# Kernel tuning notes

Hardware: AMD Instinct MI355X
Metric: run time of the kernel (lower is better)

The kernel has to match this reference:

```python
import jax, jax.numpy as jnp
import numpy as np

N_NODES = 50000
N_EDGES = 800000
N_GRAPHS = 256
F_IN = 75  # num_features_xd


def _lin_params(key, fan_in, fan_out):
    kw, kb = jax.random.split(key)
    s = 1.0 / np.sqrt(fan_in)
    W = jax.random.uniform(kw, (fan_in, fan_out), jnp.float32, -s, s)
    b = jax.random.uniform(kb, (fan_out,), jnp.float32, -s, s)
    return W, b


def setup_inputs() -> dict:
    key = jax.random.key(0)
    ks = jax.random.split(key, 8)
    x = jax.random.normal(ks[0], (N_NODES, F_IN), jnp.float32)
    edge_index = jax.random.randint(ks[1], (2, N_EDGES), 0, N_NODES, jnp.int32)
    batch = jnp.sort(jax.random.randint(ks[2], (N_NODES,), 0, N_GRAPHS, jnp.int32))
    W1, b1 = _lin_params(ks[3], F_IN, F_IN)            # conv1: 75 -> 75
    W2, b2 = _lin_params(ks[4], F_IN, 2 * F_IN)        # conv2: 75 -> 150
    W3, b3 = _lin_params(ks[5], 2 * F_IN, 4 * F_IN)    # conv3: 150 -> 300
    Wg1, bg1 = _lin_params(ks[6], 4 * F_IN, 1024)      # fc_g1: 300 -> 1024
    Wg2, bg2 = _lin_params(ks[7], 1024, 128)           # fc_g2: 1024 -> 128
    return dict(x=x, edge_index=edge_index, batch=batch,
                W1=W1, b1=b1, W2=W2, b2=b2, W3=W3, b3=b3,
                Wg1=Wg1, bg1=bg1, Wg2=Wg2, bg2=bg2)


def gcn_conv(x, W, b, src, dst, n):
    """PyG GCNConv: out = D^{-1/2}(A+I)D^{-1/2} X W + b (symmetric norm, self loops)."""
    h = x @ W                                   # [n, out]
    loop = jnp.arange(n, dtype=src.dtype)
    s = jnp.concatenate([src, loop])            # [E+n]
    d = jnp.concatenate([dst, loop])
    deg = jax.ops.segment_sum(jnp.ones(s.shape[0], x.dtype), d, num_segments=n)
    dinv = jnp.where(deg > 0, jax.lax.rsqrt(jnp.maximum(deg, 1e-12)), 0.0)
    norm = dinv[s] * dinv[d]                    # [E+n]
    out = jax.ops.segment_sum(norm[:, None] * h[s], d, num_segments=n)
    return out + b


def reference(x, edge_index, batch, W1, b1, W2, b2, W3, b3, Wg1, bg1, Wg2, bg2):
    src, dst = edge_index[0], edge_index[1]
    n = x.shape[0]
    h = jax.nn.relu(gcn_conv(x, W1, b1, src, dst, n))
    h = jax.nn.relu(gcn_conv(h, W2, b2, src, dst, n))
    h = jax.nn.relu(gcn_conv(h, W3, b3, src, dst, n))
    g = jax.ops.segment_max(h, batch, num_segments=N_GRAPHS)  # global max pool
    g = jax.nn.relu(g @ Wg1 + bg1)
    # dropout is identity in eval mode
    return g @ Wg2 + bg2
```

## Files before the change

### kernel.cpp

```cpp
#include <hip/hip_runtime.h>
#include <math.h>

#define SCAN_B 1024
#define LDST 40

typedef __attribute__((ext_vector_type(8))) short short8v;
typedef __attribute__((ext_vector_type(8))) unsigned short ushort8v;
typedef __attribute__((ext_vector_type(4))) float f32x4;

static inline int ceil_div_i(long long a, int b) { return (int)((a + b - 1) / b); }

__device__ __forceinline__ unsigned short f2bf(float x) {
    unsigned int u = __float_as_uint(x);
    u += 0x7fffu + ((u >> 16) & 1u);
    return (unsigned short)(u >> 16);
}
__device__ __forceinline__ float bf2f(unsigned short h) {
    return __uint_as_float(((unsigned int)h) << 16);
}
__device__ __forceinline__ ushort8v zero8() {
    ushort8v z;
#pragma unroll
    for (int e = 0; e < 8; e++) z[e] = 0;
    return z;
}


__global__ __launch_bounds__(256) void k_count(const int* __restrict__ dst, int E,
                                               int* __restrict__ cnt) {
    int i = blockIdx.x * blockDim.x + threadIdx.x;
    if (i < E) atomicAdd(&cnt[dst[i]], 1);
}

__global__ __launch_bounds__(256) void k_dinv(const int* __restrict__ cnt,
                                              float* __restrict__ dinv, int N) {
    int i = blockIdx.x * blockDim.x + threadIdx.x;
    if (i < N) dinv[i] = (float)(1.0 / sqrt((double)(cnt[i] + 1)));
}

__global__ __launch_bounds__(256) void k_scan1(const int* __restrict__ cnt,
                                               int* __restrict__ rowptr,
                                               int* __restrict__ bsum, int N) {
    __shared__ int s[256];
    int tid = threadIdx.x;
    int base = blockIdx.x * SCAN_B + tid * 4;
    int a0 = (base + 0 < N) ? cnt[base + 0] : 0;
    int a1 = (base + 1 < N) ? cnt[base + 1] : 0;
    int a2 = (base + 2 < N) ? cnt[base + 2] : 0;
    int a3 = (base + 3 < N) ? cnt[base + 3] : 0;
    int tsum = a0 + a1 + a2 + a3;
    s[tid] = tsum;
    __syncthreads();
    for (int off = 1; off < 256; off <<= 1) {
        int val = 0;
        if (tid >= off) val = s[tid - off];
        __syncthreads();
        if (tid >= off) s[tid] += val;
        __syncthreads();
    }
    int texcl = s[tid] - tsum;
    if (tid == 255) bsum[blockIdx.x] = s[255];
    if (base + 0 < N) rowptr[base + 0] = texcl;
    if (base + 1 < N) rowptr[base + 1] = texcl + a0;
    if (base + 2 < N) rowptr[base + 2] = texcl + a0 + a1;
    if (base + 3 < N) rowptr[base + 3] = texcl + a0 + a1 + a2;
}

__global__ __launch_bounds__(256) void k_scan2(int* __restrict__ bsum, int NB) {
    __shared__ int s[256];
    int tid = threadIdx.x;
    int v = (tid < NB) ? bsum[tid] : 0;
    s[tid] = v;
    __syncthreads();
    for (int off = 1; off < 256; off <<= 1) {
        int val = 0;
        if (tid >= off) val = s[tid - off];
        __syncthreads();
        if (tid >= off) s[tid] += val;
        __syncthreads();
    }
    if (tid < NB) bsum[tid] = s[tid] - v;
}

__global__ __launch_bounds__(256) void k_scan3(int* __restrict__ rowptr,
                                               const int* __restrict__ bsum,
                                               int* __restrict__ fill, int N, int E) {
    int i = blockIdx.x * blockDim.x + threadIdx.x;
    if (i < N) {
        int r = rowptr[i] + bsum[i >> 10];
        rowptr[i] = r;
        fill[i] = r;
    }
    if (i == 0) rowptr[N] = E;
}

__global__ __launch_bounds__(256) void k_fill(const int* __restrict__ src,
                                              const int* __restrict__ dst, int E,
                                              int* __restrict__ fill,
                                              unsigned short* __restrict__ col) {
    int base = blockIdx.x * (256 * 4) + threadIdx.x;
#pragma unroll
    for (int u = 0; u < 4; u++) {
        int e = base + u * 256;
        if (e < E) {
            int s = src[e], d = dst[e];
            int idx = atomicAdd(&fill[d], 1);
            col[idx] = (unsigned short)s;
        }
    }
}


__global__ __launch_bounds__(256) void k_xscale(const float* __restrict__ x,
                                                const float* __restrict__ dinv,
                                                unsigned short* __restrict__ xb,
                                                int N, int F, int XS) {
    int i = blockIdx.x * blockDim.x + threadIdx.x;
    int v = i / XS, c = i - v * XS;
    if (v >= N) return;
    float val = (c < F) ? dinv[v] * x[(size_t)v * F + c] : 0.f;
    xb[i] = f2bf(val);
}


template <int CHUNKS, int SLOTS, int UNR>
__global__ __launch_bounds__(256) void k_gather_s(const unsigned short* __restrict__ Xb,
                                                  const int* __restrict__ rowptr,
                                                  const unsigned short* __restrict__ col,
                                                  unsigned short* __restrict__ Th,
                                                  unsigned short* __restrict__ Tl,
                                                  int N, int XS, int KPf) {
    const int v = blockIdx.x * 4 + (threadIdx.x >> 6);
    const int lane = threadIdx.x & 63;
    if (v >= N) return;
    constexpr int VW = 8;
    const int slot = lane / CHUNKS;
    const int chunk = lane - slot * CHUNKS;
    const bool act = lane < CHUNKS * SLOTS;
    const int f0 = chunk * VW;

    float acc[VW];
#pragma unroll
    for (int u = 0; u < VW; u++) acc[u] = 0.f;
    if (slot == 0) {
        ushort8v h = *(const ushort8v*)(Xb + (size_t)v * XS + f0);
#pragma unroll
        for (int u = 0; u < VW; u++) acc[u] = bf2f(h[u]);
    }

    const int beg = rowptr[v], end = rowptr[v + 1];
    for (int jb = beg; jb < end; jb += 64) {
        const int nj = min(64, end - jb);
        int ec = 0;
        if (lane < nj) ec = (int)col[jb + lane];
        for (int e = 0; e < nj; e += SLOTS * UNR) {
            int cs[UNR];
            bool vs[UNR];
#pragma unroll
            for (int u = 0; u < UNR; u++) {
                int srcl = e + u * SLOTS + slot;
                vs[u] = act && (srcl < nj);
                cs[u] = __shfl(ec, srcl & 63);
            }
            ushort8v xv[UNR];
#pragma unroll
            for (int u = 0; u < UNR; u++) {
                xv[u] = zero8();
                if (vs[u]) xv[u] = *(const ushort8v*)(Xb + (size_t)cs[u] * XS + f0);
            }
#pragma unroll
            for (int u = 0; u < UNR; u++)
#pragma unroll
                for (int k2 = 0; k2 < VW; k2++)
                    acc[k2] += bf2f(xv[u][k2]);
        }
    }

#pragma unroll
    for (int k2 = 0; k2 < VW; k2++) {
        float t2 = acc[k2];
#pragma unroll
        for (int s2 = 1; s2 < SLOTS; s2++) t2 += __shfl(acc[k2], chunk + s2 * CHUNKS);
        acc[k2] = t2;
    }

    if (slot == 0 && f0 < KPf) {
        ushort8v h8, l8;
#pragma unroll
        for (int u = 0; u < VW; u++) {
            unsigned short hh = f2bf(acc[u]);
            h8[u] = hh;
            l8[u] = f2bf(acc[u] - bf2f(hh));
        }
        *(ushort8v*)(Th + (size_t)v * KPf + f0) = h8;
        *(ushort8v*)(Tl + (size_t)v * KPf + f0) = l8;
    }
}


__global__ __launch_bounds__(256) void k_wsplit(const float* __restrict__ W,
                                                unsigned short* __restrict__ Wth,
                                                unsigned short* __restrict__ Wtl,
                                                int K, int Fout, int KP) {
    int i = blockIdx.x * blockDim.x + threadIdx.x;
    if (i >= Fout * KP) return;
    int c = i / KP, k = i - c * KP;
    float w = (k < K) ? W[(size_t)k * Fout + c] : 0.f;
    unsigned short h = f2bf(w);
    Wth[i] = h;
    Wtl[i] = f2bf(w - bf2f(h));
}


template <int NJ2, int MODE>
__global__ __launch_bounds__(256, 4) void k_gemm_ad(
    const unsigned short* __restrict__ Ahp, const unsigned short* __restrict__ Alp, int KPf,
    const unsigned short* __restrict__ Bth, const unsigned short* __restrict__ Btl,
    const float* __restrict__ bias, const float* __restrict__ dinvp,
    unsigned short* __restrict__ Cb, int CSbf,
    const int* __restrict__ batch, float* __restrict__ G,
    int N, int KP, int Fout) {
    constexpr int CT = 16 * NJ2;
    __shared__ unsigned short sBh[CT * LDST];
    __shared__ unsigned short sBl[CT * LDST];
    __shared__ int sBatch[128];

    const int t = threadIdx.x;
    const int r0 = blockIdx.x * 128;
    const int c0 = blockIdx.y * CT;
    const int lane = t & 63;
    const int wv = t >> 6;
    const int wrow = wv * 32;
    const int l15 = lane & 15;
    const int lg = lane >> 4;
    const int nt = KP >> 5;

    if (MODE == 1 && t < 128) sBatch[t] = (r0 + t < N) ? batch[r0 + t] : -1;

    const int row0 = r0 + wrow + l15;
    const int row1 = row0 + 16;
    const bool ok0 = row0 < N;
    const bool ok1 = row1 < N;
    const unsigned short* a0h = Ahp + (size_t)row0 * KPf;
    const unsigned short* a0l = Alp + (size_t)row0 * KPf;
    const unsigned short* a1h = Ahp + (size_t)row1 * KPf;
    const unsigned short* a1l = Alp + (size_t)row1 * KPf;

    f32x4 acc[2][NJ2];
#pragma unroll
    for (int i = 0; i < 2; i++)
#pragma unroll
        for (int j = 0; j < NJ2; j++) acc[i][j] = (f32x4){0.f, 0.f, 0.f, 0.f};

    for (int tc = 0; tc < nt; ++tc) {
        const int kk = tc * 32;
        for (int idx = t; idx < CT * 4; idx += 256) {
            int brow = idx >> 2, seg = idx & 3;
            int gc = c0 + brow;
            ushort8v h = zero8(), l = zero8();
            if (gc < Fout) {
                h = *(const ushort8v*)(Bth + (size_t)gc * KP + kk + seg * 8);
                l = *(const ushort8v*)(Btl + (size_t)gc * KP + kk + seg * 8);
            }
            int boff = brow * LDST + seg * 8;
            *(ushort8v*)&sBh[boff] = h;
            *(ushort8v*)&sBl[boff] = l;
        }
        __syncthreads();

        const int gk = kk + lg * 8;
        const bool kok = gk < KPf;
        short8v A0h = (ok0 && kok) ? *(const short8v*)(a0h + gk) : (short8v)zero8();
        short8v A0l = (ok0 && kok) ? *(const short8v*)(a0l + gk) : (short8v)zero8();
        short8v A1h = (ok1 && kok) ? *(const short8v*)(a1h + gk) : (short8v)zero8();
        short8v A1l = (ok1 && kok) ? *(const short8v*)(a1l + gk) : (short8v)zero8();

#pragma unroll
        for (int j = 0; j < NJ2; j++) {
            int co = (j * 16 + l15) * LDST + lg * 8;
            short8v bh = *(const short8v*)&sBh[co];
            short8v bl = *(const short8v*)&sBl[co];
            acc[0][j] = __builtin_amdgcn_mfma_f32_16x16x32_bf16(A0l, bh, acc[0][j], 0, 0, 0);
            acc[0][j] = __builtin_amdgcn_mfma_f32_16x16x32_bf16(A0h, bl, acc[0][j], 0, 0, 0);
            acc[0][j] = __builtin_amdgcn_mfma_f32_16x16x32_bf16(A0h, bh, acc[0][j], 0, 0, 0);
            acc[1][j] = __builtin_amdgcn_mfma_f32_16x16x32_bf16(A1l, bh, acc[1][j], 0, 0, 0);
            acc[1][j] = __builtin_amdgcn_mfma_f32_16x16x32_bf16(A1h, bl, acc[1][j], 0, 0, 0);
            acc[1][j] = __builtin_amdgcn_mfma_f32_16x16x32_bf16(A1h, bh, acc[1][j], 0, 0, 0);
        }
        __syncthreads();
    }

    float drw[8];
#pragma unroll
    for (int i = 0; i < 2; i++)
#pragma unroll
        for (int q = 0; q < 4; q++) {
            int gr = r0 + wrow + i * 16 + (lane >> 4) * 4 + q;
            drw[i * 4 + q] = (gr < N) ? dinvp[gr] : 0.f;
        }

    if (MODE == 0) {
#pragma unroll
        for (int j = 0; j < NJ2; j++) {
            int gc = c0 + j * 16 + l15;
            if (gc >= CSbf) continue;
            float bv = (gc < Fout) ? bias[gc] : 0.f;
#pragma unroll
            for (int i = 0; i < 2; i++) {
                int rb = r0 + wrow + i * 16 + (lane >> 4) * 4;
#pragma unroll
                for (int q = 0; q < 4; q++) {
                    int gr = rb + q;
                    if (gr >= N) continue;
                    float dr = drw[i * 4 + q];
                    float vv = (gc < Fout) ? fmaxf(fmaf(acc[i][j][q], dr, bv), 0.f) * dr : 0.f;
                    Cb[(size_t)gr * CSbf + gc] = f2bf(vv);
                }
            }
        }
    } else {
#pragma unroll
        for (int j = 0; j < NJ2; j++) {
            int gc = c0 + j * 16 + l15;
            if (gc >= Fout) continue;
            float bv = bias[gc];
            int gcur = -1;
            float vmax = 0.f;
#pragma unroll
            for (int i = 0; i < 2; i++) {
                int lr = wrow + i * 16 + (lane >> 4) * 4;
#pragma unroll
                for (int q = 0; q < 4; q++) {
                    int g = sBatch[lr + q];
                    float vv = fmaxf(fmaf(acc[i][j][q], drw[i * 4 + q], bv), 0.f);
                    if (g < 0) continue;
                    if (g != gcur) {
                        if (gcur >= 0)
                            atomicMax((int*)&G[(size_t)gcur * Fout + gc], __float_as_int(vmax));
                        gcur = g;
                        vmax = vv;
                    } else {
                        vmax = fmaxf(vmax, vv);
                    }
                }
            }
            if (gcur >= 0) atomicMax((int*)&G[(size_t)gcur * Fout + gc], __float_as_int(vmax));
        }
    }
}


__global__ __launch_bounds__(256) void k_fc1(const float* __restrict__ A,
                                             const float* __restrict__ W,
                                             const float* __restrict__ bias,
                                             float* __restrict__ C,
                                             int M, int K, int Nout) {
    __shared__ float sA[2 * 304];
    const int t = threadIdx.x;
    const int m0 = blockIdx.x * 2;
    const int oc = blockIdx.y * 256 + t;

    for (int i = t; i < 2 * K; i += 256) {
        int r = i / K, k = i - r * K;
        sA[r * 304 + k] = (m0 + r < M) ? A[(size_t)(m0 + r) * K + k] : 0.f;
    }
    __syncthreads();

    float acc0 = 0.f, acc1 = 0.f;
    int k = 0;
    for (; k + 8 <= K; k += 8) {
        float w[8];
#pragma unroll
        for (int u = 0; u < 8; u++) w[u] = W[(size_t)(k + u) * Nout + oc];
#pragma unroll
        for (int u = 0; u < 8; u++) {
            acc0 = fmaf(sA[k + u], w[u], acc0);
            acc1 = fmaf(sA[304 + k + u], w[u], acc1);
        }
    }
    for (; k < K; k++) {
        float w = W[(size_t)k * Nout + oc];
        acc0 = fmaf(sA[k], w, acc0);
        acc1 = fmaf(sA[304 + k], w, acc1);
    }
    float bv = bias[oc];
    if (m0 < M) C[(size_t)m0 * Nout + oc] = fmaxf(acc0 + bv, 0.f);
    if (m0 + 1 < M) C[(size_t)(m0 + 1) * Nout + oc] = fmaxf(acc1 + bv, 0.f);
}


__global__ __launch_bounds__(256) void k_fc2p(const float* __restrict__ A,
                                              const float* __restrict__ W,
                                              float* __restrict__ P,
                                              int M, int K, int Nout) {
    __shared__ float sA[2 * 256];
    const int t = threadIdx.x;
    const int m0 = blockIdx.x * 2;
    const int sk = blockIdx.y;
    const int k0 = sk * 256;
    const int row = t >> 7;
    const int oc = t & 127;

    for (int i = t; i < 2 * 256; i += 256) {
        int r = i >> 8, k = i & 255;
        sA[i] = (m0 + r < M) ? A[(size_t)(m0 + r) * K + k0 + k] : 0.f;
    }
    __syncthreads();

    const float* a = sA + row * 256;
    float acc = 0.f;
    for (int k = 0; k < 256; k += 8) {
        float w[8];
#pragma unroll
        for (int u = 0; u < 8; u++) w[u] = W[(size_t)(k0 + k + u) * Nout + oc];
#pragma unroll
        for (int u = 0; u < 8; u++) acc = fmaf(a[k + u], w[u], acc);
    }
    int m = m0 + row;
    if (m < M) P[((size_t)sk * M + m) * Nout + oc] = acc;
}

__global__ __launch_bounds__(256) void k_fc2r(const float* __restrict__ P,
                                              const float* __restrict__ bias,
                                              float* __restrict__ C,
                                              int M, int Nout, int SK) {
    int i = blockIdx.x * blockDim.x + threadIdx.x;
    if (i >= M * Nout) return;
    int oc = i % Nout;
    float acc = bias[oc];
    for (int s2 = 0; s2 < SK; s2++) acc += P[(size_t)s2 * M * Nout + i];
    C[i] = acc;
}


extern "C" void kernel_launch(void* const* d_in, const int* in_sizes, int n_in,
                              void* d_out, int out_size, void* d_ws, size_t ws_size,
                              hipStream_t stream) {
    const float* x     = (const float*)d_in[0];
    const int*   ei    = (const int*)d_in[1];
    const int*   batch = (const int*)d_in[2];
    const float* W1 = (const float*)d_in[3];
    const float* b1 = (const float*)d_in[4];
    const float* W2 = (const float*)d_in[5];
    const float* b2 = (const float*)d_in[6];
    const float* W3 = (const float*)d_in[7];
    const float* b3 = (const float*)d_in[8];
    const float* Wg1 = (const float*)d_in[9];
    const float* bg1 = (const float*)d_in[10];
    const float* Wg2 = (const float*)d_in[11];
    const float* bg2 = (const float*)d_in[12];

    const int N  = in_sizes[2];
    const int E  = in_sizes[1] / 2;
    const int F1 = in_sizes[4];
    const int F2 = in_sizes[6];
    const int F3 = in_sizes[8];
    const int H1 = in_sizes[10];
    const int OC = in_sizes[12];
    const int NG = out_size / OC;
    const int FIN = in_sizes[3] / F1;

    const int KP1 = 96,  KPf1 = 80;
    const int KP3 = 160, KPf3 = 152;
    const int XS0 = 80;
    const int HS1 = 80;
    const int HS2 = 152;

    const int* src = ei;
    const int* dst = ei + E;

    char* base = (char*)d_ws;
    size_t off = 0;
    auto alloc = [&](size_t bytes) -> void* {
        void* p = base + off;
        off = (off + bytes + 255) & ~(size_t)255;
        return p;
    };
    int*   cnt    = (int*)alloc((size_t)N * 4);
    int*   fill   = (int*)alloc((size_t)N * 4);
    int*   rowptr = (int*)alloc((size_t)(N + 1) * 4);
    float* dinv   = (float*)alloc((size_t)N * 4);
    int*   bsum   = (int*)alloc(256 * 4);
    unsigned short* col = (unsigned short*)alloc((size_t)E * 2);
    unsigned short* W1th = (unsigned short*)alloc((size_t)F1 * KP1 * 2);
    unsigned short* W1tl = (unsigned short*)alloc((size_t)F1 * KP1 * 2);
    unsigned short* W2th = (unsigned short*)alloc((size_t)F2 * KP1 * 2);
    unsigned short* W2tl = (unsigned short*)alloc((size_t)F2 * KP1 * 2);
    unsigned short* W3th = (unsigned short*)alloc((size_t)F3 * KP3 * 2);
    unsigned short* W3tl = (unsigned short*)alloc((size_t)F3 * KP3 * 2);
    float* Gb  = (float*)alloc((size_t)NG * F3 * 4);
    float* g1  = (float*)alloc((size_t)NG * H1 * 4);
    float* P2  = (float*)alloc((size_t)4 * NG * OC * 4);
    unsigned short* TgH = (unsigned short*)alloc((size_t)N * KPf3 * 2);
    unsigned short* TgL = (unsigned short*)alloc((size_t)N * KPf3 * 2);
    unsigned short* Xb  = (unsigned short*)alloc((size_t)N * XS0 * 2);
    unsigned short* H1b = (unsigned short*)alloc((size_t)N * HS1 * 2);
    unsigned short* H2b = (unsigned short*)alloc((size_t)N * HS2 * 2);

    hipMemsetAsync(cnt, 0, (size_t)N * 4, stream);
    hipMemsetAsync(Gb, 0, (size_t)NG * F3 * 4, stream);

    k_count<<<ceil_div_i(E, 256), 256, 0, stream>>>(dst, E, cnt);
    k_dinv<<<ceil_div_i(N, 256), 256, 0, stream>>>(cnt, dinv, N);
    int NB = ceil_div_i(N, SCAN_B);
    k_scan1<<<NB, 256, 0, stream>>>(cnt, rowptr, bsum, N);
    k_scan2<<<1, 256, 0, stream>>>(bsum, NB);
    k_scan3<<<ceil_div_i(N, 256), 256, 0, stream>>>(rowptr, bsum, fill, N, E);
    k_fill<<<ceil_div_i(E, 1024), 256, 0, stream>>>(src, dst, E, fill, col);

    k_wsplit<<<ceil_div_i((long long)F1 * KP1, 256), 256, 0, stream>>>(W1, W1th, W1tl, FIN, F1, KP1);
    k_wsplit<<<ceil_div_i((long long)F2 * KP1, 256), 256, 0, stream>>>(W2, W2th, W2tl, F1, F2, KP1);
    k_wsplit<<<ceil_div_i((long long)F3 * KP3, 256), 256, 0, stream>>>(W3, W3th, W3tl, F2, F3, KP3);
    k_xscale<<<ceil_div_i((long long)N * XS0, 256), 256, 0, stream>>>(x, dinv, Xb, N, FIN, XS0);

    dim3 blk(256);
    int gw = ceil_div_i(N, 4);
    int gx = ceil_div_i(N, 128);

    k_gather_s<10, 6, 2><<<gw, blk, 0, stream>>>(Xb, rowptr, col, TgH, TgL, N, XS0, KPf1);
    {
        dim3 g(gx, 1);
        k_gemm_ad<6, 0><<<g, blk, 0, stream>>>(TgH, TgL, KPf1, W1th, W1tl, b1, dinv,
                                               H1b, HS1, nullptr, nullptr, N, KP1, F1);
    }
    k_gather_s<10, 6, 2><<<gw, blk, 0, stream>>>(H1b, rowptr, col, TgH, TgL, N, HS1, KPf1);
    {
        dim3 g(gx, 1);
        k_gemm_ad<10, 0><<<g, blk, 0, stream>>>(TgH, TgL, KPf1, W2th, W2tl, b2, dinv,
                                                H2b, HS2, nullptr, nullptr, N, KP1, F2);
    }
    k_gather_s<19, 3, 4><<<gw, blk, 0, stream>>>(H2b, rowptr, col, TgH, TgL, N, HS2, KPf3);
    {
        dim3 g(gx, 2);
        k_gemm_ad<10, 1><<<g, blk, 0, stream>>>(TgH, TgL, KPf3, W3th, W3tl, b3, dinv,
                                                nullptr, 0, batch, Gb, N, KP3, F3);
    }

    {
        dim3 g(ceil_div_i(NG, 2), H1 / 256);
        k_fc1<<<g, 256, 0, stream>>>(Gb, Wg1, bg1, g1, NG, F3, H1);
    }
    {
        dim3 g(ceil_div_i(NG, 2), 4);
        k_fc2p<<<g, 256, 0, stream>>>(g1, Wg2, P2, NG, H1, OC);
        k_fc2r<<<ceil_div_i((long long)NG * OC, 256), 256, 0, stream>>>(
            P2, bg2, (float*)d_out, NG, OC, 4);
    }
}
```

Baseline: 348.4 us.

## Use full-width column tiles with 64-row blocks in GCN GEMMs

The GEMM kernel now gives each block 64 rows and every output column, with each wave handling 16 rows across all column tiles, instead of 128 rows and a column split over grid.y. The third layer uses 20 column tiles in one block rather than two blocks of 10. A- and B-fragments are reused across the full width and the grid doubles in blocks, but B-tile shared-memory loads are repeated per 64 rows and accumulator register use grows for NJ2=20. The edge fill kernel also drops its 4-way per-thread unroll in favour of one edge per thread.

```diff
diff --git a/kernel.cpp b/kernel.cpp
--- a/kernel.cpp
+++ b/kernel.cpp
@@ -98,16 +98,11 @@
                                               const int* __restrict__ dst, int E,
                                               int* __restrict__ fill,
                                               unsigned short* __restrict__ col) {
-    int base = blockIdx.x * (256 * 4) + threadIdx.x;
-#pragma unroll
-    for (int u = 0; u < 4; u++) {
-        int e = base + u * 256;
-        if (e < E) {
-            int s = src[e], d = dst[e];
-            int idx = atomicAdd(&fill[d], 1);
-            col[idx] = (unsigned short)s;
-        }
-    }
+    int e = blockIdx.x * blockDim.x + threadIdx.x;
+    if (e >= E) return;
+    int s = src[e], d = dst[e];
+    int idx = atomicAdd(&fill[d], 1);
+    col[idx] = (unsigned short)s;
 }
 
 
@@ -213,7 +208,7 @@
 
 
 template <int NJ2, int MODE>
-__global__ __launch_bounds__(256, 4) void k_gemm_ad(
+__global__ __launch_bounds__(256) void k_gemm_fw(
     const unsigned short* __restrict__ Ahp, const unsigned short* __restrict__ Alp, int KPf,
     const unsigned short* __restrict__ Bth, const unsigned short* __restrict__ Btl,
     const float* __restrict__ bias, const float* __restrict__ dinvp,
@@ -223,44 +218,35 @@
     constexpr int CT = 16 * NJ2;
     __shared__ unsigned short sBh[CT * LDST];
     __shared__ unsigned short sBl[CT * LDST];
-    __shared__ int sBatch[128];
+    __shared__ int sBatch[64];
 
     const int t = threadIdx.x;
-    const int r0 = blockIdx.x * 128;
-    const int c0 = blockIdx.y * CT;
+    const int r0 = blockIdx.x * 64;
     const int lane = t & 63;
     const int wv = t >> 6;
-    const int wrow = wv * 32;
     const int l15 = lane & 15;
     const int lg = lane >> 4;
     const int nt = KP >> 5;
 
-    if (MODE == 1 && t < 128) sBatch[t] = (r0 + t < N) ? batch[r0 + t] : -1;
-
-    const int row0 = r0 + wrow + l15;
-    const int row1 = row0 + 16;
-    const bool ok0 = row0 < N;
-    const bool ok1 = row1 < N;
-    const unsigned short* a0h = Ahp + (size_t)row0 * KPf;
-    const unsigned short* a0l = Alp + (size_t)row0 * KPf;
-    const unsigned short* a1h = Ahp + (size_t)row1 * KPf;
-    const unsigned short* a1l = Alp + (size_t)row1 * KPf;
-
-    f32x4 acc[2][NJ2];
-#pragma unroll
-    for (int i = 0; i < 2; i++)
-#pragma unroll
-        for (int j = 0; j < NJ2; j++) acc[i][j] = (f32x4){0.f, 0.f, 0.f, 0.f};
+    if (MODE == 1 && t < 64) sBatch[t] = (r0 + t < N) ? batch[r0 + t] : -1;
+
+    const int row = r0 + wv * 16 + l15;
+    const bool rok = row < N;
+    const unsigned short* aH = Ahp + (size_t)row * KPf;
+    const unsigned short* aL = Alp + (size_t)row * KPf;
+
+    f32x4 acc[NJ2];
+#pragma unroll
+    for (int j = 0; j < NJ2; j++) acc[j] = (f32x4){0.f, 0.f, 0.f, 0.f};
 
     for (int tc = 0; tc < nt; ++tc) {
         const int kk = tc * 32;
         for (int idx = t; idx < CT * 4; idx += 256) {
             int brow = idx >> 2, seg = idx & 3;
-            int gc = c0 + brow;
             ushort8v h = zero8(), l = zero8();
-            if (gc < Fout) {
-                h = *(const ushort8v*)(Bth + (size_t)gc * KP + kk + seg * 8);
-                l = *(const ushort8v*)(Btl + (size_t)gc * KP + kk + seg * 8);
+            if (brow < Fout) {
+                h = *(const ushort8v*)(Bth + (size_t)brow * KP + kk + seg * 8);
+                l = *(const ushort8v*)(Btl + (size_t)brow * KP + kk + seg * 8);
             }
             int boff = brow * LDST + seg * 8;
             *(ushort8v*)&sBh[boff] = h;
@@ -269,79 +255,66 @@
         __syncthreads();
 
         const int gk = kk + lg * 8;
-        const bool kok = gk < KPf;
-        short8v A0h = (ok0 && kok) ? *(const short8v*)(a0h + gk) : (short8v)zero8();
-        short8v A0l = (ok0 && kok) ? *(const short8v*)(a0l + gk) : (short8v)zero8();
-        short8v A1h = (ok1 && kok) ? *(const short8v*)(a1h + gk) : (short8v)zero8();
-        short8v A1l = (ok1 && kok) ? *(const short8v*)(a1l + gk) : (short8v)zero8();
+        const bool kok = rok && (gk < KPf);
+        short8v Ah_ = kok ? *(const short8v*)(aH + gk) : (short8v)zero8();
+        short8v Al_ = kok ? *(const short8v*)(aL + gk) : (short8v)zero8();
 
 #pragma unroll
         for (int j = 0; j < NJ2; j++) {
             int co = (j * 16 + l15) * LDST + lg * 8;
             short8v bh = *(const short8v*)&sBh[co];
             short8v bl = *(const short8v*)&sBl[co];
-            acc[0][j] = __builtin_amdgcn_mfma_f32_16x16x32_bf16(A0l, bh, acc[0][j], 0, 0, 0);
-            acc[0][j] = __builtin_amdgcn_mfma_f32_16x16x32_bf16(A0h, bl, acc[0][j], 0, 0, 0);
-            acc[0][j] = __builtin_amdgcn_mfma_f32_16x16x32_bf16(A0h, bh, acc[0][j], 0, 0, 0);
-            acc[1][j] = __builtin_amdgcn_mfma_f32_16x16x32_bf16(A1l, bh, acc[1][j], 0, 0, 0);
-            acc[1][j] = __builtin_amdgcn_mfma_f32_16x16x32_bf16(A1h, bl, acc[1][j], 0, 0, 0);
-            acc[1][j] = __builtin_amdgcn_mfma_f32_16x16x32_bf16(A1h, bh, acc[1][j], 0, 0, 0);
+            acc[j] = __builtin_amdgcn_mfma_f32_16x16x32_bf16(Al_, bh, acc[j], 0, 0, 0);
+            acc[j] = __builtin_amdgcn_mfma_f32_16x16x32_bf16(Ah_, bl, acc[j], 0, 0, 0);
+            acc[j] = __builtin_amdgcn_mfma_f32_16x16x32_bf16(Ah_, bh, acc[j], 0, 0, 0);
         }
         __syncthreads();
     }
 
-    float drw[8];
-#pragma unroll
-    for (int i = 0; i < 2; i++)
-#pragma unroll
-        for (int q = 0; q < 4; q++) {
-            int gr = r0 + wrow + i * 16 + (lane >> 4) * 4 + q;
-            drw[i * 4 + q] = (gr < N) ? dinvp[gr] : 0.f;
-        }
+    float drw[4];
+#pragma unroll
+    for (int q = 0; q < 4; q++) {
+        int gr = r0 + wv * 16 + (lane >> 4) * 4 + q;
+        drw[q] = (gr < N) ? dinvp[gr] : 0.f;
+    }
 
     if (MODE == 0) {
 #pragma unroll
         for (int j = 0; j < NJ2; j++) {
-            int gc = c0 + j * 16 + l15;
+            int gc = j * 16 + l15;
             if (gc >= CSbf) continue;
             float bv = (gc < Fout) ? bias[gc] : 0.f;
-#pragma unroll
-            for (int i = 0; i < 2; i++) {
-                int rb = r0 + wrow + i * 16 + (lane >> 4) * 4;
-#pragma unroll
-                for (int q = 0; q < 4; q++) {
-                    int gr = rb + q;
-                    if (gr >= N) continue;
-                    float dr = drw[i * 4 + q];
-                    float vv = (gc < Fout) ? fmaxf(fmaf(acc[i][j][q], dr, bv), 0.f) * dr : 0.f;
-                    Cb[(size_t)gr * CSbf + gc] = f2bf(vv);
-                }
+            int rb = r0 + wv * 16 + (lane >> 4) * 4;
+#pragma unroll
+            for (int q = 0; q < 4; q++) {
+                int gr = rb + q;
+                if (gr >= N) continue;
+                float dr = drw[q];
+                float vv = (gc < Fout) ? fmaxf(fmaf(acc[j][q], dr, bv), 0.f) * dr : 0.f;
+                Cb[(size_t)gr * CSbf + gc] = f2bf(vv);
             }
         }
     } else {
 #pragma unroll
         for (int j = 0; j < NJ2; j++) {
-            int gc = c0 + j * 16 + l15;
+            int gc = j * 16 + l15;
             if (gc >= Fout) continue;
             float bv = bias[gc];
+            int lr = wv * 16 + (lane >> 4) * 4;
             int gcur = -1;
             float vmax = 0.f;
 #pragma unroll
-            for (int i = 0; i < 2; i++) {
-                int lr = wrow + i * 16 + (lane >> 4) * 4;
-#pragma unroll
-                for (int q = 0; q < 4; q++) {
-                    int g = sBatch[lr + q];
-                    float vv = fmaxf(fmaf(acc[i][j][q], drw[i * 4 + q], bv), 0.f);
-                    if (g < 0) continue;
-                    if (g != gcur) {
-                        if (gcur >= 0)
-                            atomicMax((int*)&G[(size_t)gcur * Fout + gc], __float_as_int(vmax));
-                        gcur = g;
-                        vmax = vv;
-                    } else {
-                        vmax = fmaxf(vmax, vv);
-                    }
+            for (int q = 0; q < 4; q++) {
+                int g = sBatch[lr + q];
+                float vv = fmaxf(fmaf(acc[j][q], drw[q], bv), 0.f);
+                if (g < 0) continue;
+                if (g != gcur) {
+                    if (gcur >= 0)
+                        atomicMax((int*)&G[(size_t)gcur * Fout + gc], __float_as_int(vmax));
+                    gcur = g;
+                    vmax = vv;
+                } else {
+                    vmax = fmaxf(vmax, vv);
                 }
             }
             if (gcur >= 0) atomicMax((int*)&G[(size_t)gcur * Fout + gc], __float_as_int(vmax));
@@ -506,7 +479,7 @@
     k_scan1<<<NB, 256, 0, stream>>>(cnt, rowptr, bsum, N);
     k_scan2<<<1, 256, 0, stream>>>(bsum, NB);
     k_scan3<<<ceil_div_i(N, 256), 256, 0, stream>>>(rowptr, bsum, fill, N, E);
-    k_fill<<<ceil_div_i(E, 1024), 256, 0, stream>>>(src, dst, E, fill, col);
+    k_fill<<<ceil_div_i(E, 256), 256, 0, stream>>>(src, dst, E, fill, col);
 
     k_wsplit<<<ceil_div_i((long long)F1 * KP1, 256), 256, 0, stream>>>(W1, W1th, W1tl, FIN, F1, KP1);
     k_wsplit<<<ceil_div_i((long long)F2 * KP1, 256), 256, 0, stream>>>(W2, W2th, W2tl, F1, F2, KP1);
@@ -515,26 +488,17 @@
 
     dim3 blk(256);
     int gw = ceil_div_i(N, 4);
-    int gx = ceil_div_i(N, 128);
+    int gx = ceil_div_i(N, 64);
 
     k_gather_s<10, 6, 2><<<gw, blk, 0, stream>>>(Xb, rowptr, col, TgH, TgL, N, XS0, KPf1);
-    {
-        dim3 g(gx, 1);
-        k_gemm_ad<6, 0><<<g, blk, 0, stream>>>(TgH, TgL, KPf1, W1th, W1tl, b1, dinv,
-                                               H1b, HS1, nullptr, nullptr, N, KP1, F1);
-    }
+    k_gemm_fw<6, 0><<<gx, blk, 0, stream>>>(TgH, TgL, KPf1, W1th, W1tl, b1, dinv,
+                                            H1b, HS1, nullptr, nullptr, N, KP1, F1);
     k_gather_s<10, 6, 2><<<gw, blk, 0, stream>>>(H1b, rowptr, col, TgH, TgL, N, HS1, KPf1);
-    {
-        dim3 g(gx, 1);
-        k_gemm_ad<10, 0><<<g, blk, 0, stream>>>(TgH, TgL, KPf1, W2th, W2tl, b2, dinv,
-                                                H2b, HS2, nullptr, nullptr, N, KP1, F2);
-    }
+    k_gemm_fw<10, 0><<<gx, blk, 0, stream>>>(TgH, TgL, KPf1, W2th, W2tl, b2, dinv,
+                                             H2b, HS2, nullptr, nullptr, N, KP1, F2);
     k_gather_s<19, 3, 4><<<gw, blk, 0, stream>>>(H2b, rowptr, col, TgH, TgL, N, HS2, KPf3);
-    {
-        dim3 g(gx, 2);
-        k_gemm_ad<10, 1><<<g, blk, 0, stream>>>(TgH, TgL, KPf3, W3th, W3tl, b3, dinv,
-                                                nullptr, 0, batch, Gb, N, KP3, F3);
-    }
+    k_gemm_fw<20, 1><<<gx, blk, 0, stream>>>(TgH, TgL, KPf3, W3th, W3tl, b3, dinv,
+                                             nullptr, 0, batch, Gb, N, KP3, F3);
 
     {
         dim3 g(ceil_div_i(NG, 2), H1 / 256);
```

Result: slower. 377.6 us (+8.4%).

## Remap GEMM blocks per XCD and split fill kernel to one edge per thread

Applied to the files above, without the earlier changes.

The GEMM grid is flattened to 1D and block indices are remapped so that consecutive logical tiles (row tile, column tile) land on the same XCD. The aim is better L2 reuse of A rows and B tiles on MI355X's chiplet layout. The edge-fill kernel now launches one thread per edge instead of four edges per thread, which gives more parallelism for the atomics. The max-pool epilogue now flushes an atomicMax per 16-row half instead of once per column, which adds some atomics but shortens the dependency chain.

```diff
diff --git a/kernel.cpp b/kernel.cpp
--- a/kernel.cpp
+++ b/kernel.cpp
@@ -98,16 +98,11 @@
                                               const int* __restrict__ dst, int E,
                                               int* __restrict__ fill,
                                               unsigned short* __restrict__ col) {
-    int base = blockIdx.x * (256 * 4) + threadIdx.x;
-#pragma unroll
-    for (int u = 0; u < 4; u++) {
-        int e = base + u * 256;
-        if (e < E) {
-            int s = src[e], d = dst[e];
-            int idx = atomicAdd(&fill[d], 1);
-            col[idx] = (unsigned short)s;
-        }
-    }
+    int e = blockIdx.x * blockDim.x + threadIdx.x;
+    if (e >= E) return;
+    int s = src[e], d = dst[e];
+    int idx = atomicAdd(&fill[d], 1);
+    col[idx] = (unsigned short)s;
 }
 
 
@@ -212,22 +207,32 @@
 }
 
 
-template <int NJ2, int MODE>
+template <int NJ2, int GY, int MODE>
 __global__ __launch_bounds__(256, 4) void k_gemm_ad(
     const unsigned short* __restrict__ Ahp, const unsigned short* __restrict__ Alp, int KPf,
     const unsigned short* __restrict__ Bth, const unsigned short* __restrict__ Btl,
     const float* __restrict__ bias, const float* __restrict__ dinvp,
     unsigned short* __restrict__ Cb, int CSbf,
     const int* __restrict__ batch, float* __restrict__ G,
-    int N, int KP, int Fout) {
+    int N, int KP, int Fout, int nwg) {
     constexpr int CT = 16 * NJ2;
     __shared__ unsigned short sBh[CT * LDST];
     __shared__ unsigned short sBl[CT * LDST];
     __shared__ int sBatch[128];
 
+    {
+    }
+    const int b = blockIdx.x;
+    const int q = nwg >> 3, r8 = nwg & 7;
+    const int xcd = b & 7, idx = b >> 3;
+    const int L = (xcd < r8) ? xcd * (q + 1) + idx
+                             : r8 * (q + 1) + (xcd - r8) * q + idx;
+    const int rx = L / GY;
+    const int cy = L - rx * GY;
+
     const int t = threadIdx.x;
-    const int r0 = blockIdx.x * 128;
-    const int c0 = blockIdx.y * CT;
+    const int r0 = rx * 128;
+    const int c0 = cy * CT;
     const int lane = t & 63;
     const int wv = t >> 6;
     const int wrow = wv * 32;
@@ -254,8 +259,8 @@
 
     for (int tc = 0; tc < nt; ++tc) {
         const int kk = tc * 32;
-        for (int idx = t; idx < CT * 4; idx += 256) {
-            int brow = idx >> 2, seg = idx & 3;
+        for (int idx2 = t; idx2 < CT * 4; idx2 += 256) {
+            int brow = idx2 >> 2, seg = idx2 & 3;
             int gc = c0 + brow;
             ushort8v h = zero8(), l = zero8();
             if (gc < Fout) {
@@ -294,9 +299,9 @@
 #pragma unroll
     for (int i = 0; i < 2; i++)
 #pragma unroll
-        for (int q = 0; q < 4; q++) {
-            int gr = r0 + wrow + i * 16 + (lane >> 4) * 4 + q;
-            drw[i * 4 + q] = (gr < N) ? dinvp[gr] : 0.f;
+        for (int q2 = 0; q2 < 4; q2++) {
+            int gr = r0 + wrow + i * 16 + (lane >> 4) * 4 + q2;
+            drw[i * 4 + q2] = (gr < N) ? dinvp[gr] : 0.f;
         }
 
     if (MODE == 0) {
@@ -309,11 +314,11 @@
             for (int i = 0; i < 2; i++) {
                 int rb = r0 + wrow + i * 16 + (lane >> 4) * 4;
 #pragma unroll
-                for (int q = 0; q < 4; q++) {
-                    int gr = rb + q;
+                for (int q2 = 0; q2 < 4; q2++) {
+                    int gr = rb + q2;
                     if (gr >= N) continue;
-                    float dr = drw[i * 4 + q];
-                    float vv = (gc < Fout) ? fmaxf(fmaf(acc[i][j][q], dr, bv), 0.f) * dr : 0.f;
+                    float dr = drw[i * 4 + q2];
+                    float vv = (gc < Fout) ? fmaxf(fmaf(acc[i][j][q2], dr, bv), 0.f) * dr : 0.f;
                     Cb[(size_t)gr * CSbf + gc] = f2bf(vv);
                 }
             }
@@ -324,15 +329,15 @@
             int gc = c0 + j * 16 + l15;
             if (gc >= Fout) continue;
             float bv = bias[gc];
-            int gcur = -1;
-            float vmax = 0.f;
 #pragma unroll
             for (int i = 0; i < 2; i++) {
                 int lr = wrow + i * 16 + (lane >> 4) * 4;
-#pragma unroll
-                for (int q = 0; q < 4; q++) {
-                    int g = sBatch[lr + q];
-                    float vv = fmaxf(fmaf(acc[i][j][q], drw[i * 4 + q], bv), 0.f);
+                int gcur = -1;
+                float vmax = 0.f;
+#pragma unroll
+                for (int q2 = 0; q2 < 4; q2++) {
+                    int g = sBatch[lr + q2];
+                    float vv = fmaxf(fmaf(acc[i][j][q2], drw[i * 4 + q2], bv), 0.f);
                     if (g < 0) continue;
                     if (g != gcur) {
                         if (gcur >= 0)
@@ -343,8 +348,8 @@
                         vmax = fmaxf(vmax, vv);
                     }
                 }
+                if (gcur >= 0) atomicMax((int*)&G[(size_t)gcur * Fout + gc], __float_as_int(vmax));
             }
-            if (gcur >= 0) atomicMax((int*)&G[(size_t)gcur * Fout + gc], __float_as_int(vmax));
         }
     }
 }
@@ -506,7 +511,7 @@
     k_scan1<<<NB, 256, 0, stream>>>(cnt, rowptr, bsum, N);
     k_scan2<<<1, 256, 0, stream>>>(bsum, NB);
     k_scan3<<<ceil_div_i(N, 256), 256, 0, stream>>>(rowptr, bsum, fill, N, E);
-    k_fill<<<ceil_div_i(E, 1024), 256, 0, stream>>>(src, dst, E, fill, col);
+    k_fill<<<ceil_div_i(E, 256), 256, 0, stream>>>(src, dst, E, fill, col);
 
     k_wsplit<<<ceil_div_i((long long)F1 * KP1, 256), 256, 0, stream>>>(W1, W1th, W1tl, FIN, F1, KP1);
     k_wsplit<<<ceil_div_i((long long)F2 * KP1, 256), 256, 0, stream>>>(W2, W2th, W2tl, F1, F2, KP1);
@@ -518,23 +523,14 @@
     int gx = ceil_div_i(N, 128);
 
     k_gather_s<10, 6, 2><<<gw, blk, 0, stream>>>(Xb, rowptr, col, TgH, TgL, N, XS0, KPf1);
-    {
-        dim3 g(gx, 1);
-        k_gemm_ad<6, 0><<<g, blk, 0, stream>>>(TgH, TgL, KPf1, W1th, W1tl, b1, dinv,
-                                               H1b, HS1, nullptr, nullptr, N, KP1, F1);
-    }
+    k_gemm_ad<6, 1, 0><<<gx, blk, 0, stream>>>(TgH, TgL, KPf1, W1th, W1tl, b1, dinv,
+                                               H1b, HS1, nullptr, nullptr, N, KP1, F1, gx);
     k_gather_s<10, 6, 2><<<gw, blk, 0, stream>>>(H1b, rowptr, col, TgH, TgL, N, HS1, KPf1);
-    {
-        dim3 g(gx, 1);
-        k_gemm_ad<10, 0><<<g, blk, 0, stream>>>(TgH, TgL, KPf1, W2th, W2tl, b2, dinv,
-                                                H2b, HS2, nullptr, nullptr, N, KP1, F2);
-    }
+    k_gemm_ad<10, 1, 0><<<gx, blk, 0, stream>>>(TgH, TgL, KPf1, W2th, W2tl, b2, dinv,
+                                                H2b, HS2, nullptr, nullptr, N, KP1, F2, gx);
     k_gather_s<19, 3, 4><<<gw, blk, 0, stream>>>(H2b, rowptr, col, TgH, TgL, N, HS2, KPf3);
-    {
-        dim3 g(gx, 2);
-        k_gemm_ad<10, 1><<<g, blk, 0, stream>>>(TgH, TgL, KPf3, W3th, W3tl, b3, dinv,
-                                                nullptr, 0, batch, Gb, N, KP3, F3);
-    }
+    k_gemm_ad<10, 2, 1><<<gx * 2, blk, 0, stream>>>(TgH, TgL, KPf3, W3th, W3tl, b3, dinv,
+                                                    nullptr, 0, batch, Gb, N, KP3, F3, gx * 2);
 
     {
         dim3 g(ceil_div_i(NG, 2), H1 / 256);
```

After: 358.3 us. +2.8%, slower.
